# Performance work log

Measured on AMD Instinct MI355X. Metric: run time of the kernel, lower is better.

The kernel has to match this reference:

```python
import jax, jax.numpy as jnp
import numpy as np

EPS = 1e-5

def _conv_bn_relu(x, w, gamma, beta):
    # x: [B, C, N], w: [O, C] (1x1 conv, no bias)
    y = jnp.einsum('oc,bcn->bon', w, x)
    # BatchNorm1d in training mode: per-channel stats over (B, N)
    mean = jnp.mean(y, axis=(0, 2), keepdims=True)
    var = jnp.var(y, axis=(0, 2), keepdims=True)
    yhat = (y - mean) * jax.lax.rsqrt(var + EPS)
    return jax.nn.relu(gamma[None, :, None] * yhat + beta[None, :, None])


def setup_inputs() -> dict:
    key = jax.random.key(0)
    ks = jax.random.split(key, 8)
    B, C, N, Cr = 4, 256, 4096, 32
    x = jax.random.normal(ks[0], (B, C, N), dtype=jnp.float32)
    w1 = jax.random.normal(ks[1], (Cr, C), dtype=jnp.float32) * (1.0 / np.sqrt(C))
    w2 = jax.random.normal(ks[2], (Cr, C), dtype=jnp.float32) * (1.0 / np.sqrt(C))
    w3 = jax.random.normal(ks[3], (C, C), dtype=jnp.float32) * (1.0 / np.sqrt(C))
    g1 = 1.0 + 0.1 * jax.random.normal(ks[4], (Cr,), dtype=jnp.float32)
    b1 = 0.1 * jax.random.normal(ks[5], (Cr,), dtype=jnp.float32)
    g2 = 1.0 + 0.1 * jax.random.normal(ks[6], (Cr,), dtype=jnp.float32)
    b2 = 0.1 * jax.random.normal(ks[7], (Cr,), dtype=jnp.float32)
    g3 = jnp.ones((C,), dtype=jnp.float32)
    b3 = jnp.zeros((C,), dtype=jnp.float32)
    return {'x': x, 'w1': w1, 'w2': w2, 'w3': w3,
            'g1': g1, 'b1': b1, 'g2': g2, 'b2': b2, 'g3': g3, 'b3': b3}


def reference(x, w1, w2, w3, g1, b1, g2, b2, g3, b3):
    # a: [B, N, Cr] (queries), k: [B, Cr, N] (keys)
    a = _conv_bn_relu(x, w1, g1, b1).transpose(0, 2, 1)
    k = _conv_bn_relu(x, w2, g2, b2)
    # s[b, n, m] = softmax_m(sum_c a[b,n,c] * k[b,c,m])
    s = jax.nn.softmax(jnp.einsum('bnc,bcm->bnm', a, k), axis=-1)
    d = _conv_bn_relu(x, w3, g3, b3)  # [B, C, N]
    # out = x + d @ s^T : out[b,c,m] = sum_n d[b,c,n] * s[m,n]
    out = x + jnp.einsum('bcn,bmn->bcm', d, s)
    return out
```

## Files before the change

kernel.cpp:

```cpp
#include <hip/hip_runtime.h>
#include <cstddef>
#include <cstdint>

#define B_ 4
#define C_ 256
#define N_ 4096
#define KF_OFF_B  ((size_t)1024 * 1024)
#define DF_OFF_B  ((size_t)2 * 1024 * 1024)
#define SUM_OFF_B ((size_t)10 * 1024 * 1024)
#define ML_OFF_B  (SUM_OFF_B + 1280 * 4)
#define XH_OFF_B  (ML_OFF_B + 524288)
#define XL_OFF_B  (XH_OFF_B + (size_t)8 * 1024 * 1024)
#define WH_OFF_B  (XL_OFF_B + (size_t)8 * 1024 * 1024)
#define WL_OFF_B  (WH_OFF_B + 163840)
#define LOG2E 1.4426950408889634f

typedef unsigned short bfraw;
typedef __attribute__((ext_vector_type(8))) short short8;
typedef __attribute__((ext_vector_type(4))) float float4v;
typedef __attribute__((ext_vector_type(4))) bfraw bfraw4;

__device__ inline bfraw f2bf(float f) {
    union { float f; uint32_t u; } c; c.f = f;
    uint32_t u = c.u;
    u += 0x7fffu + ((u >> 16) & 1u);
    return (bfraw)(u >> 16);
}
__device__ inline float bf2f(bfraw h) {
    union { uint32_t u; float f; } c; c.u = ((uint32_t)h) << 16;
    return c.f;
}
#if __has_builtin(__builtin_amdgcn_exp2f)
__device__ inline float EXP2(float x) { return __builtin_amdgcn_exp2f(x); }
#else
__device__ inline float EXP2(float x) { return exp2f(x); }
#endif
__device__ inline uint32_t pack2(float a, float b) {
    union { float f; uint32_t u; } ca, cb; ca.f = a; cb.f = b;
#if __has_builtin(__builtin_amdgcn_perm)
    return __builtin_amdgcn_perm(cb.u + 0x8000u, ca.u + 0x8000u, 0x07060302u);
#else
    return ((ca.u + 0x8000u) >> 16) | ((cb.u + 0x8000u) & 0xffff0000u);
#endif
}

__global__ __launch_bounds__(256) void prep_kernel(
    const float* __restrict__ x,
    const float* __restrict__ w1, const float* __restrict__ w2,
    const float* __restrict__ w3, uint8_t* __restrict__ wsb)
{
    __shared__ float Ls[64][65];
    if (blockIdx.x >= 1024) {
        int bid = blockIdx.x - 1024;
        if (bid == 0) {
            float* sums = (float*)(wsb + SUM_OFF_B);
            for (int i = threadIdx.x; i < 640; i += 256) sums[i] = 0.f;
        }
        bfraw* wh = (bfraw*)(wsb + WH_OFF_B);
        bfraw* wl = (bfraw*)(wsb + WL_OFF_B);
        int idx4 = (bid * 256 + threadIdx.x) * 4;
        int ch = idx4 >> 8, k = idx4 & 255;
        const float* wr = (ch < 32) ? (w1 + ch * C_)
                          : (ch < 64) ? (w2 + (ch - 32) * C_)
                                      : (w3 + (ch - 64) * C_);
        float4 v = *(const float4*)&wr[k];
        float va[4] = {v.x, v.y, v.z, v.w};
        bfraw4 h, l;
#pragma unroll
        for (int j = 0; j < 4; ++j) {
            h[j] = f2bf(va[j]);
            l[j] = f2bf(va[j] - bf2f(h[j]));
        }
        *(bfraw4*)&wh[idx4] = h;
        *(bfraw4*)&wl[idx4] = l;
        return;
    }
    bfraw* xh = (bfraw*)(wsb + XH_OFF_B);
    bfraw* xl = (bfraw*)(wsb + XL_OFF_B);
    const int id = blockIdx.x;
    const int b  = id >> 8;
    const int c0 = ((id >> 6) & 3) << 6;
    const int n0 = (id & 63) << 6;
    const int t  = threadIdx.x;
    {
        int cl = t >> 4, nc = (t & 15) << 2;
#pragma unroll
        for (int i = 0; i < 4; ++i) {
            float4 v = *(const float4*)&x[((size_t)b * C_ + c0 + cl + i * 16) * N_ + n0 + nc];
            Ls[cl + i * 16][nc + 0] = v.x;
            Ls[cl + i * 16][nc + 1] = v.y;
            Ls[cl + i * 16][nc + 2] = v.z;
            Ls[cl + i * 16][nc + 3] = v.w;
        }
    }
    __syncthreads();
    int nl = t >> 2, seg = t & 3;
    bfraw hb[16], lb[16];
#pragma unroll
    for (int j = 0; j < 16; ++j) {
        float v = Ls[seg * 16 + j][nl];
        bfraw h = f2bf(v);
        hb[j] = h;
        lb[j] = f2bf(v - bf2f(h));
    }
    size_t base = ((size_t)b * N_ + n0 + nl) * 256 + c0 + seg * 16;
    *(short8*)&xh[base]     = *(short8*)&hb[0];
    *(short8*)&xh[base + 8] = *(short8*)&hb[8];
    *(short8*)&xl[base]     = *(short8*)&lb[0];
    *(short8*)&xl[base + 8] = *(short8*)&lb[8];
}

__global__ __launch_bounds__(256, 2) void ygemm_kernel(uint8_t* __restrict__ wsb)
{
    const bfraw* xh = (const bfraw*)(wsb + XH_OFF_B);
    const bfraw* xl = (const bfraw*)(wsb + XL_OFF_B);
    const bfraw* wh = (const bfraw*)(wsb + WH_OFF_B);
    const bfraw* wl = (const bfraw*)(wsb + WL_OFF_B);
    bfraw* qf  = (bfraw*)wsb;
    bfraw* kfp = (bfraw*)(wsb + KF_OFF_B);
    bfraw* dfp = (bfraw*)(wsb + DF_OFF_B);
    float* sums  = (float*)(wsb + SUM_OFF_B);
    float* sumsq = sums + 320;
    __shared__ float redS[4][64], redQ[4][64];
    __shared__ bfraw Td[4][64 * 40];

    const int bx = blockIdx.x;
    const int by = blockIdx.y;
    const int b  = bx >> 5;
    const int n0 = (bx << 7) & (N_ - 1);
    const int t = threadIdx.x, w = t >> 6, l = t & 63, lq = l & 15, lg = l >> 4;
    const int nw = n0 + w * 32;

    float4v acc[4][2];
#pragma unroll
    for (int i = 0; i < 4; ++i)
#pragma unroll
        for (int j = 0; j < 2; ++j) acc[i][j] = (float4v){0.f, 0.f, 0.f, 0.f};

#pragma unroll 2
    for (int s = 0; s < 8; ++s) {
        const int k0 = s * 32;
        short8 ah[4], al[4], bh[2], bl[2];
#pragma unroll
        for (int ct = 0; ct < 4; ++ct) {
            size_t off = (size_t)(by * 64 + ct * 16 + lq) * 256 + k0 + lg * 8;
            ah[ct] = *(const short8*)&wh[off];
            al[ct] = *(const short8*)&wl[off];
        }
#pragma unroll
        for (int nt = 0; nt < 2; ++nt) {
            size_t off = ((size_t)b * N_ + nw + nt * 16 + lq) * 256 + k0 + lg * 8;
            bh[nt] = *(const short8*)&xh[off];
            bl[nt] = *(const short8*)&xl[off];
        }
#pragma unroll
        for (int ct = 0; ct < 4; ++ct)
#pragma unroll
            for (int nt = 0; nt < 2; ++nt) {
                acc[ct][nt] = __builtin_amdgcn_mfma_f32_16x16x32_bf16(ah[ct], bh[nt], acc[ct][nt], 0, 0, 0);
                acc[ct][nt] = __builtin_amdgcn_mfma_f32_16x16x32_bf16(al[ct], bh[nt], acc[ct][nt], 0, 0, 0);
                acc[ct][nt] = __builtin_amdgcn_mfma_f32_16x16x32_bf16(ah[ct], bl[nt], acc[ct][nt], 0, 0, 0);
            }
    }
#pragma unroll
    for (int ct = 0; ct < 4; ++ct) {
        float sv[4], qv[4];
#pragma unroll
        for (int r = 0; r < 4; ++r) {
            float a0 = acc[ct][0][r], a1 = acc[ct][1][r];
            sv[r] = a0 + a1;
            qv[r] = a0 * a0 + a1 * a1;
#pragma unroll
            for (int m = 1; m < 16; m <<= 1) {
                sv[r] += __shfl_xor(sv[r], m);
                qv[r] += __shfl_xor(qv[r], m);
            }
        }
        if (lq == 0) {
#pragma unroll
            for (int r = 0; r < 4; ++r) {
                redS[w][ct * 16 + lg * 4 + r] = sv[r];
                redQ[w][ct * 16 + lg * 4 + r] = qv[r];
            }
        }
    }
    __syncthreads();
    if (t < 64) {
        float s = redS[0][t] + redS[1][t] + redS[2][t] + redS[3][t];
        float q = redQ[0][t] + redQ[1][t] + redQ[2][t] + redQ[3][t];
        atomicAdd(&sums[by * 64 + t], s);
        atomicAdd(&sumsq[by * 64 + t], q);
    }
    if (by == 0) {
#pragma unroll
        for (int ct = 0; ct < 4; ++ct)
#pragma unroll
            for (int nt = 0; nt < 2; ++nt) {
                int n = nw + nt * 16 + lq;
                int c0 = ct * 16 + lg * 4;
                bfraw4 v;
#pragma unroll
                for (int r = 0; r < 4; ++r) v[r] = f2bf(acc[ct][nt][r]);
                size_t addr = ((size_t)(b << 8) + (n >> 4)) * 512
                            + (size_t)(((n & 15) | (((c0 >> 3) & 3) << 4)) << 3) + (c0 & 7);
                if (c0 < 32) *(bfraw4*)&qf[addr] = v;
                else         *(bfraw4*)&kfp[addr] = v;
            }
    } else {
#pragma unroll
        for (int ct = 0; ct < 4; ++ct)
#pragma unroll
            for (int nt = 0; nt < 2; ++nt)
#pragma unroll
                for (int r = 0; r < 4; ++r) {
                    int cl = ct * 16 + lg * 4 + r;
                    int nl = nt * 16 + lq;
                    Td[w][cl * 40 + nl] = f2bf(acc[ct][nt][r]);
                }
        __syncthreads();
#pragma unroll
        for (int ctl = 0; ctl < 4; ++ctl) {
            short8 vv = *(const short8*)&Td[w][(ctl * 16 + (l & 15)) * 40 + (l >> 4) * 8];
            size_t addr = (((size_t)(b << 4) + (by - 1) * 4 + ctl) * 128 + (nw >> 5)) * 512
                        + (size_t)l * 8;
            *(short8*)&dfp[addr] = vv;
        }
    }
}

__device__ inline void bn_coef(const float* __restrict__ sums,
                               const float* __restrict__ g1, const float* __restrict__ b1,
                               const float* __restrict__ g2, const float* __restrict__ b2,
                               const float* __restrict__ g3, const float* __restrict__ b3,
                               int ch, float& sc, float& bi)
{
    const float inv = 1.0f / (float)(B_ * N_);
    float mean = sums[ch] * inv;
    float var  = sums[320 + ch] * inv - mean * mean;
    float g, bb;
    if (ch < 32)      { g = g1[ch];      bb = b1[ch]; }
    else if (ch < 64) { g = g2[ch - 32]; bb = b2[ch - 32]; }
    else              { g = g3[ch - 64]; bb = b3[ch - 64]; }
    sc = g * rsqrtf(var + 1e-5f);
    bi = bb - sc * mean;
    if (ch < 32) { sc *= LOG2E; bi *= LOG2E; }
}

__global__ __launch_bounds__(256) void affine_kernel(
    uint8_t* __restrict__ wsb,
    const float* __restrict__ g1, const float* __restrict__ b1,
    const float* __restrict__ g2, const float* __restrict__ b2,
    const float* __restrict__ g3, const float* __restrict__ b3)
{
    bfraw* base = (bfraw*)wsb;
    const float* sums = (const float*)(wsb + SUM_OFF_B);
    size_t i8 = ((size_t)blockIdx.x * 256 + threadIdx.x) * 8;
    bfraw4 v0 = *(bfraw4*)&base[i8];
    bfraw4 v1 = *(bfraw4*)&base[i8 + 4];
    if (i8 < 1048576) {
        int ch0 = (((int)(i8 >> 7)) & 3) * 8 + ((i8 < 524288) ? 0 : 32);
        float sa[8], ca[8];
#pragma unroll
        for (int j = 0; j < 8; ++j)
            bn_coef(sums, g1, b1, g2, b2, g3, b3, ch0 + j, sa[j], ca[j]);
#pragma unroll
        for (int j = 0; j < 4; ++j) {
            v0[j] = f2bf(fmaxf(0.f, fmaf(sa[j],     bf2f(v0[j]), ca[j])));
            v1[j] = f2bf(fmaxf(0.f, fmaf(sa[j + 4], bf2f(v1[j]), ca[j + 4])));
        }
    } else {
        size_t rel = i8 - 1048576;
        int ch = 64 + (((int)(rel >> 16)) & 15) * 16 + (((int)(rel >> 3)) & 15);
        float s, b;
        bn_coef(sums, g1, b1, g2, b2, g3, b3, ch, s, b);
#pragma unroll
        for (int j = 0; j < 4; ++j) {
            v0[j] = f2bf(fmaxf(0.f, fmaf(s, bf2f(v0[j]), b)));
            v1[j] = f2bf(fmaxf(0.f, fmaf(s, bf2f(v1[j]), b)));
        }
    }
    *(bfraw4*)&base[i8] = v0;
    *(bfraw4*)&base[i8 + 4] = v1;
}

__global__ __launch_bounds__(512, 2) void flash_kernel(
    const float* __restrict__ x, const uint8_t* __restrict__ wsb,
    float* __restrict__ out)
{
    const bfraw* qf  = (const bfraw*)wsb;
    const bfraw* kfp = (const bfraw*)(wsb + KF_OFF_B);
    const bfraw* dfp = (const bfraw*)(wsb + DF_OFF_B);
    __shared__ bfraw Pl[2][64 * 256];
    __shared__ float lsh[2][64];

    const int id  = blockIdx.x;
    const int b   = id & 3;
    const int n0q = (id >> 2) << 6;
    const int tid = threadIdx.x;
    const int w   = tid >> 6;
    const int l   = tid & 63;
    const int lq  = l & 15;
    const int lg  = l >> 4;
    const int sw  = lq & 7;
    const int qt_s   = w >> 1;
    const int ks_loc = w & 1;
    const int ctg0 = w;
    const int ctg1 = 8 + w;

    const short8 qfrag = *(const short8*)&qf[((size_t)(b * 256 + (n0q >> 4) + qt_s)) * 512 + l * 8];
    const float4v zv = {-16.f, -16.f, -16.f, -16.f};

    float ps = 0.f;
    float4v acc[2][4];
#pragma unroll
    for (int i = 0; i < 2; ++i)
#pragma unroll
        for (int j = 0; j < 4; ++j) acc[i][j] = (float4v){0.f, 0.f, 0.f, 0.f};

    short8 dfr[2][8];
#pragma unroll
    for (int ch = 0; ch < 8; ++ch) {
        dfr[0][ch] = *(const short8*)&dfp[(((size_t)(b * 16 + ctg0)) * 128 + ch) * 512 + l * 8];
        dfr[1][ch] = *(const short8*)&dfp[(((size_t)(b * 16 + ctg1)) * 128 + ch) * 512 + l * 8];
    }
    short8 kfr[8];
#pragma unroll
    for (int kt = 0; kt < 8; ++kt)
        kfr[kt] = *(const short8*)&kfp[((size_t)(b * 256 + ks_loc * 8 + kt)) * 512 + l * 8];

    const int qrow = qt_s * 16 + lq;
    for (int it = 0; it < 16; ++it) {
        const int ib = it & 1;
        const int nit = (it + 1) & 15;
        float4v st[8];
#pragma unroll
        for (int kt = 0; kt < 8; ++kt)
            st[kt] = __builtin_amdgcn_mfma_f32_16x16x32_bf16(kfr[kt], qfrag, zv, 0, 0, 0);
#pragma unroll
        for (int kt = 0; kt < 8; ++kt)
            kfr[kt] = *(const short8*)&kfp[((size_t)(b * 256 + nit * 16 + ks_loc * 8 + kt)) * 512 + l * 8];
#pragma unroll
        for (int kt = 0; kt < 8; ++kt) {
            float e0 = EXP2(st[kt][0]);
            float e1 = EXP2(st[kt][1]);
            float e2 = EXP2(st[kt][2]);
            float e3 = EXP2(st[kt][3]);
            ps += (e0 + e1) + (e2 + e3);
            uint2 pd = {pack2(e0, e1), pack2(e2, e3)};
            int g = (2 * (ks_loc * 8 + kt) + (lg >> 1)) ^ sw;
            *(uint2*)&Pl[ib][qrow * 256 + g * 8 + (lg & 1) * 4] = pd;
        }
        __syncthreads();
#pragma unroll
        for (int ch = 0; ch < 8; ++ch) {
            short8 bfr[4];
            int g = (ch * 4 + lg) ^ sw;
#pragma unroll
            for (int qt = 0; qt < 4; ++qt)
                bfr[qt] = *(const short8*)&Pl[ib][(qt * 16 + lq) * 256 + g * 8];
            __builtin_amdgcn_s_setprio(1);
#pragma unroll
            for (int qt = 0; qt < 4; ++qt) {
                acc[0][qt] = __builtin_amdgcn_mfma_f32_16x16x32_bf16(dfr[0][ch], bfr[qt], acc[0][qt], 0, 0, 0);
                acc[1][qt] = __builtin_amdgcn_mfma_f32_16x16x32_bf16(dfr[1][ch], bfr[qt], acc[1][qt], 0, 0, 0);
            }
            __builtin_amdgcn_s_setprio(0);
            dfr[0][ch] = *(const short8*)&dfp[(((size_t)(b * 16 + ctg0)) * 128 + nit * 8 + ch) * 512 + l * 8];
            dfr[1][ch] = *(const short8*)&dfp[(((size_t)(b * 16 + ctg1)) * 128 + nit * 8 + ch) * 512 + l * 8];
        }
    }
    ps += __shfl_xor(ps, 16);
    ps += __shfl_xor(ps, 32);
    if (lg == 0) lsh[ks_loc][qrow] = ps;
    __syncthreads();
    float inv[4];
#pragma unroll
    for (int qt = 0; qt < 4; ++qt) {
        int qg = qt * 16 + lq;
        inv[qt] = 1.0f / (lsh[0][qg] + lsh[1][qg]);
    }
#pragma unroll
    for (int ct = 0; ct < 2; ++ct) {
        int ctg = ct ? ctg1 : ctg0;
#pragma unroll
        for (int r = 0; r < 4; ++r) {
            int c = ctg * 16 + lg * 4 + r;
            size_t base = ((size_t)b * C_ + c) * N_ + n0q;
#pragma unroll
            for (int qt = 0; qt < 4; ++qt) {
                size_t idx = base + qt * 16 + lq;
                out[idx] = x[idx] + acc[ct][qt][r] * inv[qt];
            }
        }
    }
}

extern "C" void kernel_launch(void* const* d_in, const int* in_sizes, int n_in,
                              void* d_out, int out_size, void* d_ws, size_t ws_size,
                              hipStream_t stream) {
    (void)in_sizes; (void)n_in; (void)out_size; (void)ws_size;
    const float* x  = (const float*)d_in[0];
    const float* w1 = (const float*)d_in[1];
    const float* w2 = (const float*)d_in[2];
    const float* w3 = (const float*)d_in[3];
    const float* g1 = (const float*)d_in[4];
    const float* b1 = (const float*)d_in[5];
    const float* g2 = (const float*)d_in[6];
    const float* b2 = (const float*)d_in[7];
    const float* g3 = (const float*)d_in[8];
    const float* b3 = (const float*)d_in[9];
    uint8_t* wsb = (uint8_t*)d_ws;
    float* outp = (float*)d_out;

    prep_kernel<<<1104, 256, 0, stream>>>(x, w1, w2, w3, wsb);
    ygemm_kernel<<<dim3(128, 5), 256, 0, stream>>>(wsb);
    affine_kernel<<<2560, 256, 0, stream>>>(wsb, g1, b1, g2, b2, g3, b3);
    flash_kernel<<<256, 512, 0, stream>>>(x, wsb, outp);
}
```

Before: 174.2 us.

## Warp-specialize flash kernel into score producers and PV-MMA consumer warps

Splits the 8 waves of the flash kernel into 4 producer waves that compute QK scores, exponentiate, and write P tiles to shared memory, and 4 consumer waves that run the P·D MFMAs one iteration behind. The goal is to overlap exp/pack work with the matrix multiplies instead of running them serially. Each consumer wave now holds a 4x4 accumulator set and streams its D fragments at half depth. The trade-off is higher register pressure in consumer waves and load imbalance between the roles. The unroll pragma on the conv kernel's K loop is also removed.

```diff
diff --git a/kernel.cpp b/kernel.cpp
--- a/kernel.cpp
+++ b/kernel.cpp
@@ -137,7 +137,6 @@
 #pragma unroll
         for (int j = 0; j < 2; ++j) acc[i][j] = (float4v){0.f, 0.f, 0.f, 0.f};
 
-#pragma unroll 2
     for (int s = 0; s < 8; ++s) {
         const int k0 = s * 32;
         short8 ah[4], al[4], bh[2], bl[2];
@@ -291,7 +290,7 @@
     const bfraw* kfp = (const bfraw*)(wsb + KF_OFF_B);
     const bfraw* dfp = (const bfraw*)(wsb + DF_OFF_B);
     __shared__ bfraw Pl[2][64 * 256];
-    __shared__ float lsh[2][64];
+    __shared__ float lsh[64];
 
     const int id  = blockIdx.x;
     const int b   = id & 3;
@@ -302,94 +301,125 @@
     const int lq  = l & 15;
     const int lg  = l >> 4;
     const int sw  = lq & 7;
-    const int qt_s   = w >> 1;
-    const int ks_loc = w & 1;
-    const int ctg0 = w;
-    const int ctg1 = 8 + w;
-
-    const short8 qfrag = *(const short8*)&qf[((size_t)(b * 256 + (n0q >> 4) + qt_s)) * 512 + l * 8];
     const float4v zv = {-16.f, -16.f, -16.f, -16.f};
 
+    short8 qfrag;
+    short8 kfr[8];
     float ps = 0.f;
-    float4v acc[2][4];
-#pragma unroll
-    for (int i = 0; i < 2; ++i)
-#pragma unroll
-        for (int j = 0; j < 4; ++j) acc[i][j] = (float4v){0.f, 0.f, 0.f, 0.f};
-
-    short8 dfr[2][8];
-#pragma unroll
-    for (int ch = 0; ch < 8; ++ch) {
-        dfr[0][ch] = *(const short8*)&dfp[(((size_t)(b * 16 + ctg0)) * 128 + ch) * 512 + l * 8];
-        dfr[1][ch] = *(const short8*)&dfp[(((size_t)(b * 16 + ctg1)) * 128 + ch) * 512 + l * 8];
-    }
-    short8 kfr[8];
-#pragma unroll
-    for (int kt = 0; kt < 8; ++kt)
-        kfr[kt] = *(const short8*)&kfp[((size_t)(b * 256 + ks_loc * 8 + kt)) * 512 + l * 8];
-
-    const int qrow = qt_s * 16 + lq;
-    for (int it = 0; it < 16; ++it) {
-        const int ib = it & 1;
-        const int nit = (it + 1) & 15;
-        float4v st[8];
+    int qrow = 0;
+    const int wp = w & 3;
+    float4v acc[4][4];
+    short8 dfr[4][4];
+
+    if (w < 4) {
+        qrow = w * 16 + lq;
+        qfrag = *(const short8*)&qf[((size_t)(b * 256 + (n0q >> 4) + w)) * 512 + l * 8];
 #pragma unroll
         for (int kt = 0; kt < 8; ++kt)
-            st[kt] = __builtin_amdgcn_mfma_f32_16x16x32_bf16(kfr[kt], qfrag, zv, 0, 0, 0);
-#pragma unroll
-        for (int kt = 0; kt < 8; ++kt)
-            kfr[kt] = *(const short8*)&kfp[((size_t)(b * 256 + nit * 16 + ks_loc * 8 + kt)) * 512 + l * 8];
-#pragma unroll
-        for (int kt = 0; kt < 8; ++kt) {
-            float e0 = EXP2(st[kt][0]);
-            float e1 = EXP2(st[kt][1]);
-            float e2 = EXP2(st[kt][2]);
-            float e3 = EXP2(st[kt][3]);
-            ps += (e0 + e1) + (e2 + e3);
-            uint2 pd = {pack2(e0, e1), pack2(e2, e3)};
-            int g = (2 * (ks_loc * 8 + kt) + (lg >> 1)) ^ sw;
-            *(uint2*)&Pl[ib][qrow * 256 + g * 8 + (lg & 1) * 4] = pd;
+            kfr[kt] = *(const short8*)&kfp[((size_t)(b * 256 + kt)) * 512 + l * 8];
+    } else {
+#pragma unroll
+        for (int i = 0; i < 4; ++i)
+#pragma unroll
+            for (int j = 0; j < 4; ++j) acc[i][j] = (float4v){0.f, 0.f, 0.f, 0.f};
+#pragma unroll
+        for (int i = 0; i < 4; ++i)
+#pragma unroll
+            for (int c = 0; c < 4; ++c)
+                dfr[i][c] = *(const short8*)&dfp[(((size_t)(b * 16 + wp + 4 * i)) * 128 + c) * 512 + l * 8];
+    }
+
+    for (int t = 0; t <= 16; ++t) {
+        if (w < 4) {
+            if (t < 16) {
+                const int ib = t & 1;
+                float4v st[8];
+#pragma unroll
+                for (int kt = 0; kt < 8; ++kt)
+                    st[kt] = __builtin_amdgcn_mfma_f32_16x16x32_bf16(kfr[kt], qfrag, zv, 0, 0, 0);
+#pragma unroll
+                for (int kt = 0; kt < 8; ++kt)
+                    kfr[kt] = *(const short8*)&kfp[((size_t)(b * 256 + t * 16 + 8 + kt)) * 512 + l * 8];
+#pragma unroll
+                for (int kt = 0; kt < 8; ++kt) {
+                    float e0 = EXP2(st[kt][0]);
+                    float e1 = EXP2(st[kt][1]);
+                    float e2 = EXP2(st[kt][2]);
+                    float e3 = EXP2(st[kt][3]);
+                    ps += (e0 + e1) + (e2 + e3);
+                    uint2 pd = {pack2(e0, e1), pack2(e2, e3)};
+                    int g = (2 * kt + (lg >> 1)) ^ sw;
+                    *(uint2*)&Pl[ib][qrow * 256 + g * 8 + (lg & 1) * 4] = pd;
+                }
+#pragma unroll
+                for (int kt = 0; kt < 8; ++kt)
+                    st[kt] = __builtin_amdgcn_mfma_f32_16x16x32_bf16(kfr[kt], qfrag, zv, 0, 0, 0);
+#pragma unroll
+                for (int kt = 0; kt < 8; ++kt)
+                    kfr[kt] = *(const short8*)&kfp[((size_t)(b * 256 + (((t + 1) & 15) * 16) + kt)) * 512 + l * 8];
+#pragma unroll
+                for (int kt = 0; kt < 8; ++kt) {
+                    float e0 = EXP2(st[kt][0]);
+                    float e1 = EXP2(st[kt][1]);
+                    float e2 = EXP2(st[kt][2]);
+                    float e3 = EXP2(st[kt][3]);
+                    ps += (e0 + e1) + (e2 + e3);
+                    uint2 pd = {pack2(e0, e1), pack2(e2, e3)};
+                    int g = (2 * (kt + 8) + (lg >> 1)) ^ sw;
+                    *(uint2*)&Pl[ib][qrow * 256 + g * 8 + (lg & 1) * 4] = pd;
+                }
+            }
+        } else {
+            if (t >= 1) {
+                const int wd = t - 1;
+                const int ib = wd & 1;
+#pragma unroll
+                for (int ch = 0; ch < 8; ++ch) {
+                    short8 bfr[4];
+                    int g = (ch * 4 + lg) ^ sw;
+#pragma unroll
+                    for (int qt = 0; qt < 4; ++qt)
+                        bfr[qt] = *(const short8*)&Pl[ib][(qt * 16 + lq) * 256 + g * 8];
+                    __builtin_amdgcn_s_setprio(1);
+#pragma unroll
+                    for (int i = 0; i < 4; ++i)
+#pragma unroll
+                        for (int qt = 0; qt < 4; ++qt)
+                            acc[i][qt] = __builtin_amdgcn_mfma_f32_16x16x32_bf16(dfr[i][ch & 3], bfr[qt], acc[i][qt], 0, 0, 0);
+                    __builtin_amdgcn_s_setprio(0);
+                    int rwd = (ch < 4) ? wd : ((wd + 1) & 15);
+                    int rch = (ch < 4) ? (ch + 4) : (ch - 4);
+#pragma unroll
+                    for (int i = 0; i < 4; ++i)
+                        dfr[i][ch & 3] = *(const short8*)&dfp[(((size_t)(b * 16 + wp + 4 * i)) * 128 + rwd * 8 + rch) * 512 + l * 8];
+                }
+            }
         }
         __syncthreads();
-#pragma unroll
-        for (int ch = 0; ch < 8; ++ch) {
-            short8 bfr[4];
-            int g = (ch * 4 + lg) ^ sw;
-#pragma unroll
-            for (int qt = 0; qt < 4; ++qt)
-                bfr[qt] = *(const short8*)&Pl[ib][(qt * 16 + lq) * 256 + g * 8];
-            __builtin_amdgcn_s_setprio(1);
-#pragma unroll
-            for (int qt = 0; qt < 4; ++qt) {
-                acc[0][qt] = __builtin_amdgcn_mfma_f32_16x16x32_bf16(dfr[0][ch], bfr[qt], acc[0][qt], 0, 0, 0);
-                acc[1][qt] = __builtin_amdgcn_mfma_f32_16x16x32_bf16(dfr[1][ch], bfr[qt], acc[1][qt], 0, 0, 0);
-            }
-            __builtin_amdgcn_s_setprio(0);
-            dfr[0][ch] = *(const short8*)&dfp[(((size_t)(b * 16 + ctg0)) * 128 + nit * 8 + ch) * 512 + l * 8];
-            dfr[1][ch] = *(const short8*)&dfp[(((size_t)(b * 16 + ctg1)) * 128 + nit * 8 + ch) * 512 + l * 8];
-        }
-    }
-    ps += __shfl_xor(ps, 16);
-    ps += __shfl_xor(ps, 32);
-    if (lg == 0) lsh[ks_loc][qrow] = ps;
+    }
+    if (w < 4) {
+        ps += __shfl_xor(ps, 16);
+        ps += __shfl_xor(ps, 32);
+        if (lg == 0) lsh[qrow] = ps;
+    }
     __syncthreads();
-    float inv[4];
-#pragma unroll
-    for (int qt = 0; qt < 4; ++qt) {
-        int qg = qt * 16 + lq;
-        inv[qt] = 1.0f / (lsh[0][qg] + lsh[1][qg]);
-    }
-#pragma unroll
-    for (int ct = 0; ct < 2; ++ct) {
-        int ctg = ct ? ctg1 : ctg0;
-#pragma unroll
-        for (int r = 0; r < 4; ++r) {
-            int c = ctg * 16 + lg * 4 + r;
-            size_t base = ((size_t)b * C_ + c) * N_ + n0q;
-#pragma unroll
-            for (int qt = 0; qt < 4; ++qt) {
-                size_t idx = base + qt * 16 + lq;
-                out[idx] = x[idx] + acc[ct][qt][r] * inv[qt];
+    if (w >= 4) {
+        float inv[4];
+#pragma unroll
+        for (int qt = 0; qt < 4; ++qt)
+            inv[qt] = 1.0f / lsh[qt * 16 + lq];
+#pragma unroll
+        for (int i = 0; i < 4; ++i) {
+            int ctg = wp + 4 * i;
+#pragma unroll
+            for (int r = 0; r < 4; ++r) {
+                int c = ctg * 16 + lg * 4 + r;
+                size_t base = ((size_t)b * C_ + c) * N_ + n0q;
+#pragma unroll
+                for (int qt = 0; qt < 4; ++qt) {
+                    size_t idx = base + qt * 16 + lq;
+                    out[idx] = x[idx] + acc[i][qt][r] * inv[qt];
+                }
             }
         }
     }
```

Measured after the change: 175.8 us. About the same (+0.9%).

## Fuse BN affine into GEMM kernel via cooperative grid sync

Applied to the files above, without the earlier changes.

Merges the 1x1-conv GEMM and the BatchNorm affine+ReLU pass into one cooperative kernel. Each block now computes 80 channels instead of 64, so the grid shrinks to 512 blocks and all blocks can be resident at once. A grid-wide sync waits for the global channel statistics, and the normalization is then applied to the accumulators still held in registers before the bf16 results are written. This drops the separate affine kernel's read and write of the intermediates and one launch. In exchange it adds a grid barrier and a wider per-thread accumulator tile, which raises register pressure.

```diff
diff --git a/kernel.cpp b/kernel.cpp
--- a/kernel.cpp
+++ b/kernel.cpp
@@ -1,6 +1,9 @@
 #include <hip/hip_runtime.h>
+#include <hip/hip_cooperative_groups.h>
 #include <cstddef>
 #include <cstdint>
+
+namespace cg = cooperative_groups;
 
 #define B_ 4
 #define C_ 256
@@ -108,124 +111,6 @@
     *(short8*)&xh[base + 8] = *(short8*)&hb[8];
     *(short8*)&xl[base]     = *(short8*)&lb[0];
     *(short8*)&xl[base + 8] = *(short8*)&lb[8];
-}
-
-__global__ __launch_bounds__(256, 2) void ygemm_kernel(uint8_t* __restrict__ wsb)
-{
-    const bfraw* xh = (const bfraw*)(wsb + XH_OFF_B);
-    const bfraw* xl = (const bfraw*)(wsb + XL_OFF_B);
-    const bfraw* wh = (const bfraw*)(wsb + WH_OFF_B);
-    const bfraw* wl = (const bfraw*)(wsb + WL_OFF_B);
-    bfraw* qf  = (bfraw*)wsb;
-    bfraw* kfp = (bfraw*)(wsb + KF_OFF_B);
-    bfraw* dfp = (bfraw*)(wsb + DF_OFF_B);
-    float* sums  = (float*)(wsb + SUM_OFF_B);
-    float* sumsq = sums + 320;
-    __shared__ float redS[4][64], redQ[4][64];
-    __shared__ bfraw Td[4][64 * 40];
-
-    const int bx = blockIdx.x;
-    const int by = blockIdx.y;
-    const int b  = bx >> 5;
-    const int n0 = (bx << 7) & (N_ - 1);
-    const int t = threadIdx.x, w = t >> 6, l = t & 63, lq = l & 15, lg = l >> 4;
-    const int nw = n0 + w * 32;
-
-    float4v acc[4][2];
-#pragma unroll
-    for (int i = 0; i < 4; ++i)
-#pragma unroll
-        for (int j = 0; j < 2; ++j) acc[i][j] = (float4v){0.f, 0.f, 0.f, 0.f};
-
-#pragma unroll 2
-    for (int s = 0; s < 8; ++s) {
-        const int k0 = s * 32;
-        short8 ah[4], al[4], bh[2], bl[2];
-#pragma unroll
-        for (int ct = 0; ct < 4; ++ct) {
-            size_t off = (size_t)(by * 64 + ct * 16 + lq) * 256 + k0 + lg * 8;
-            ah[ct] = *(const short8*)&wh[off];
-            al[ct] = *(const short8*)&wl[off];
-        }
-#pragma unroll
-        for (int nt = 0; nt < 2; ++nt) {
-            size_t off = ((size_t)b * N_ + nw + nt * 16 + lq) * 256 + k0 + lg * 8;
-            bh[nt] = *(const short8*)&xh[off];
-            bl[nt] = *(const short8*)&xl[off];
-        }
-#pragma unroll
-        for (int ct = 0; ct < 4; ++ct)
-#pragma unroll
-            for (int nt = 0; nt < 2; ++nt) {
-                acc[ct][nt] = __builtin_amdgcn_mfma_f32_16x16x32_bf16(ah[ct], bh[nt], acc[ct][nt], 0, 0, 0);
-                acc[ct][nt] = __builtin_amdgcn_mfma_f32_16x16x32_bf16(al[ct], bh[nt], acc[ct][nt], 0, 0, 0);
-                acc[ct][nt] = __builtin_amdgcn_mfma_f32_16x16x32_bf16(ah[ct], bl[nt], acc[ct][nt], 0, 0, 0);
-            }
-    }
-#pragma unroll
-    for (int ct = 0; ct < 4; ++ct) {
-        float sv[4], qv[4];
-#pragma unroll
-        for (int r = 0; r < 4; ++r) {
-            float a0 = acc[ct][0][r], a1 = acc[ct][1][r];
-            sv[r] = a0 + a1;
-            qv[r] = a0 * a0 + a1 * a1;
-#pragma unroll
-            for (int m = 1; m < 16; m <<= 1) {
-                sv[r] += __shfl_xor(sv[r], m);
-                qv[r] += __shfl_xor(qv[r], m);
-            }
-        }
-        if (lq == 0) {
-#pragma unroll
-            for (int r = 0; r < 4; ++r) {
-                redS[w][ct * 16 + lg * 4 + r] = sv[r];
-                redQ[w][ct * 16 + lg * 4 + r] = qv[r];
-            }
-        }
-    }
-    __syncthreads();
-    if (t < 64) {
-        float s = redS[0][t] + redS[1][t] + redS[2][t] + redS[3][t];
-        float q = redQ[0][t] + redQ[1][t] + redQ[2][t] + redQ[3][t];
-        atomicAdd(&sums[by * 64 + t], s);
-        atomicAdd(&sumsq[by * 64 + t], q);
-    }
-    if (by == 0) {
-#pragma unroll
-        for (int ct = 0; ct < 4; ++ct)
-#pragma unroll
-            for (int nt = 0; nt < 2; ++nt) {
-                int n = nw + nt * 16 + lq;
-                int c0 = ct * 16 + lg * 4;
-                bfraw4 v;
-#pragma unroll
-                for (int r = 0; r < 4; ++r) v[r] = f2bf(acc[ct][nt][r]);
-                size_t addr = ((size_t)(b << 8) + (n >> 4)) * 512
-                            + (size_t)(((n & 15) | (((c0 >> 3) & 3) << 4)) << 3) + (c0 & 7);
-                if (c0 < 32) *(bfraw4*)&qf[addr] = v;
-                else         *(bfraw4*)&kfp[addr] = v;
-            }
-    } else {
-#pragma unroll
-        for (int ct = 0; ct < 4; ++ct)
-#pragma unroll
-            for (int nt = 0; nt < 2; ++nt)
-#pragma unroll
-                for (int r = 0; r < 4; ++r) {
-                    int cl = ct * 16 + lg * 4 + r;
-                    int nl = nt * 16 + lq;
-                    Td[w][cl * 40 + nl] = f2bf(acc[ct][nt][r]);
-                }
-        __syncthreads();
-#pragma unroll
-        for (int ctl = 0; ctl < 4; ++ctl) {
-            short8 vv = *(const short8*)&Td[w][(ctl * 16 + (l & 15)) * 40 + (l >> 4) * 8];
-            size_t addr = (((size_t)(b << 4) + (by - 1) * 4 + ctl) * 128 + (nw >> 5)) * 512
-                        + (size_t)l * 8;
-            *(short8*)&dfp[addr] = vv;
-        }
-    }
 }
 
 __device__ inline void bn_coef(const float* __restrict__ sums,
@@ -246,41 +131,128 @@
     if (ch < 32) { sc *= LOG2E; bi *= LOG2E; }
 }
 
-__global__ __launch_bounds__(256) void affine_kernel(
+__global__ __launch_bounds__(256, 2) void ygemm_fused_kernel(
     uint8_t* __restrict__ wsb,
     const float* __restrict__ g1, const float* __restrict__ b1,
     const float* __restrict__ g2, const float* __restrict__ b2,
     const float* __restrict__ g3, const float* __restrict__ b3)
 {
-    bfraw* base = (bfraw*)wsb;
-    const float* sums = (const float*)(wsb + SUM_OFF_B);
-    size_t i8 = ((size_t)blockIdx.x * 256 + threadIdx.x) * 8;
-    bfraw4 v0 = *(bfraw4*)&base[i8];
-    bfraw4 v1 = *(bfraw4*)&base[i8 + 4];
-    if (i8 < 1048576) {
-        int ch0 = (((int)(i8 >> 7)) & 3) * 8 + ((i8 < 524288) ? 0 : 32);
-        float sa[8], ca[8];
-#pragma unroll
-        for (int j = 0; j < 8; ++j)
-            bn_coef(sums, g1, b1, g2, b2, g3, b3, ch0 + j, sa[j], ca[j]);
-#pragma unroll
-        for (int j = 0; j < 4; ++j) {
-            v0[j] = f2bf(fmaxf(0.f, fmaf(sa[j],     bf2f(v0[j]), ca[j])));
-            v1[j] = f2bf(fmaxf(0.f, fmaf(sa[j + 4], bf2f(v1[j]), ca[j + 4])));
-        }
-    } else {
-        size_t rel = i8 - 1048576;
-        int ch = 64 + (((int)(rel >> 16)) & 15) * 16 + (((int)(rel >> 3)) & 15);
-        float s, b;
-        bn_coef(sums, g1, b1, g2, b2, g3, b3, ch, s, b);
-#pragma unroll
-        for (int j = 0; j < 4; ++j) {
-            v0[j] = f2bf(fmaxf(0.f, fmaf(s, bf2f(v0[j]), b)));
-            v1[j] = f2bf(fmaxf(0.f, fmaf(s, bf2f(v1[j]), b)));
-        }
-    }
-    *(bfraw4*)&base[i8] = v0;
-    *(bfraw4*)&base[i8 + 4] = v1;
+    const bfraw* xh = (const bfraw*)(wsb + XH_OFF_B);
+    const bfraw* xl = (const bfraw*)(wsb + XL_OFF_B);
+    const bfraw* wh = (const bfraw*)(wsb + WH_OFF_B);
+    const bfraw* wl = (const bfraw*)(wsb + WL_OFF_B);
+    bfraw* qf  = (bfraw*)wsb;
+    bfraw* kfp = (bfraw*)(wsb + KF_OFF_B);
+    bfraw* dfp = (bfraw*)(wsb + DF_OFF_B);
+    float* sums  = (float*)(wsb + SUM_OFF_B);
+    float* sumsq = sums + 320;
+    __shared__ float redS[4][80], redQ[4][80];
+    __shared__ bfraw Td[4][16 * 40];
+
+    const int id = blockIdx.x;
+    const int by = id >> 7;
+    const int bx = id & 127;
+    const int b  = bx >> 5;
+    const int n0 = (bx & 31) << 7;
+    const int t = threadIdx.x, w = t >> 6, l = t & 63, lq = l & 15, lg = l >> 4;
+    const int nw = n0 + w * 32;
+
+    float4v acc[5][2];
+#pragma unroll
+    for (int i = 0; i < 5; ++i)
+#pragma unroll
+        for (int j = 0; j < 2; ++j) acc[i][j] = (float4v){0.f, 0.f, 0.f, 0.f};
+
+    for (int s = 0; s < 8; ++s) {
+        const int k0 = s * 32;
+        short8 ah[5], al[5], bh[2], bl[2];
+#pragma unroll
+        for (int ct = 0; ct < 5; ++ct) {
+            size_t off = (size_t)((by * 5 + ct) * 16 + lq) * 256 + k0 + lg * 8;
+            ah[ct] = *(const short8*)&wh[off];
+            al[ct] = *(const short8*)&wl[off];
+        }
+#pragma unroll
+        for (int nt = 0; nt < 2; ++nt) {
+            size_t off = ((size_t)b * N_ + nw + nt * 16 + lq) * 256 + k0 + lg * 8;
+            bh[nt] = *(const short8*)&xh[off];
+            bl[nt] = *(const short8*)&xl[off];
+        }
+#pragma unroll
+        for (int ct = 0; ct < 5; ++ct)
+#pragma unroll
+            for (int nt = 0; nt < 2; ++nt) {
+                acc[ct][nt] = __builtin_amdgcn_mfma_f32_16x16x32_bf16(ah[ct], bh[nt], acc[ct][nt], 0, 0, 0);
+                acc[ct][nt] = __builtin_amdgcn_mfma_f32_16x16x32_bf16(al[ct], bh[nt], acc[ct][nt], 0, 0, 0);
+                acc[ct][nt] = __builtin_amdgcn_mfma_f32_16x16x32_bf16(ah[ct], bl[nt], acc[ct][nt], 0, 0, 0);
+            }
+    }
+#pragma unroll
+    for (int ct = 0; ct < 5; ++ct) {
+        float sv[4], qv[4];
+#pragma unroll
+        for (int r = 0; r < 4; ++r) {
+            float a0 = acc[ct][0][r], a1 = acc[ct][1][r];
+            sv[r] = a0 + a1;
+            qv[r] = a0 * a0 + a1 * a1;
+#pragma unroll
+            for (int m = 1; m < 16; m <<= 1) {
+                sv[r] += __shfl_xor(sv[r], m);
+                qv[r] += __shfl_xor(qv[r], m);
+            }
+        }
+        if (lq == 0) {
+#pragma unroll
+            for (int r = 0; r < 4; ++r) {
+                redS[w][ct * 16 + lg * 4 + r] = sv[r];
+                redQ[w][ct * 16 + lg * 4 + r] = qv[r];
+            }
+        }
+    }
+    __syncthreads();
+    if (t < 80) {
+        float s = redS[0][t] + redS[1][t] + redS[2][t] + redS[3][t];
+        float q = redQ[0][t] + redQ[1][t] + redQ[2][t] + redQ[3][t];
+        atomicAdd(&sums[by * 80 + t], s);
+        atomicAdd(&sumsq[by * 80 + t], q);
+    }
+
+    cg::this_grid().sync();
+
+#pragma unroll
+    for (int ct = 0; ct < 5; ++ct) {
+        const int ctp = by * 5 + ct;
+        const int c0 = ctp * 16 + lg * 4;
+        float sc[4], bi[4];
+#pragma unroll
+        for (int r = 0; r < 4; ++r)
+            bn_coef(sums, g1, b1, g2, b2, g3, b3, c0 + r, sc[r], bi[r]);
+        if (ctp < 4) {
+#pragma unroll
+            for (int nt = 0; nt < 2; ++nt) {
+                int n = nw + nt * 16 + lq;
+                bfraw4 v;
+#pragma unroll
+                for (int r = 0; r < 4; ++r)
+                    v[r] = f2bf(fmaxf(0.f, fmaf(sc[r], acc[ct][nt][r], bi[r])));
+                size_t addr = ((size_t)(b << 8) + (n >> 4)) * 512
+                            + (size_t)(((n & 15) | (((c0 >> 3) & 3) << 4)) << 3) + (c0 & 7);
+                if (c0 < 32) *(bfraw4*)&qf[addr] = v;
+                else         *(bfraw4*)&kfp[addr] = v;
+            }
+        } else {
+#pragma unroll
+            for (int nt = 0; nt < 2; ++nt)
+#pragma unroll
+                for (int r = 0; r < 4; ++r)
+                    Td[w][(lg * 4 + r) * 40 + nt * 16 + lq] =
+                        f2bf(fmaxf(0.f, fmaf(sc[r], acc[ct][nt][r], bi[r])));
+            short8 vv = *(const short8*)&Td[w][(l & 15) * 40 + (l >> 4) * 8];
+            size_t addr = (((size_t)(b << 4) + (ctp - 4)) * 128 + (nw >> 5)) * 512
+                        + (size_t)l * 8;
+            *(short8*)&dfp[addr] = vv;
+        }
+    }
 }
 
 __global__ __launch_bounds__(512, 2) void flash_kernel(
@@ -413,7 +385,11 @@
     float* outp = (float*)d_out;
 
     prep_kernel<<<1104, 256, 0, stream>>>(x, w1, w2, w3, wsb);
-    ygemm_kernel<<<dim3(128, 5), 256, 0, stream>>>(wsb);
-    affine_kernel<<<2560, 256, 0, stream>>>(wsb, g1, b1, g2, b2, g3, b3);
+    {
+        void* args[] = {(void*)&wsb, (void*)&g1, (void*)&b1, (void*)&g2,
+                        (void*)&b2, (void*)&g3, (void*)&b3};
+        hipLaunchCooperativeKernel(reinterpret_cast<void*>(ygemm_fused_kernel),
+                                   dim3(512), dim3(256), args, 0, stream);
+    }
     flash_kernel<<<256, 512, 0, stream>>>(x, wsb, outp);
 }
```

After: 230.5 us. 1.32x slower.
